# Kernel tuning notes

Hardware: AMD Instinct MI355X
Metric: run time of the kernel (lower is better)

## Reference

```python
import jax, jax.numpy as jnp
import numpy as np

EPS = 1e-6  # module eps (unused in forward math, kept for fidelity)


def _relative_transform(rot_a, trans_a, rot_b, trans_b):
    # rel_rot = R_a @ R_b^T ; rel_trans = t_a - rel_rot @ t_b
    rel_rot = jnp.einsum('bij,bkj->bik', rot_a, rot_b)          # [B,3,3]
    rel_trans = trans_a - jnp.einsum('bij,bj->bi', rel_rot, trans_b)  # [B,3]
    return rel_rot, rel_trans


def setup_inputs() -> dict:
    key = jax.random.key(0)
    ks = jax.random.split(key, 9)
    B, N = 8, 4096
    return {
        'pred_rot': jax.random.normal(ks[0], (B, 3, 3), jnp.float32),
        'pred_trans': jax.random.normal(ks[1], (B, 3), jnp.float32),
        'ctx_hyp_rot': jax.random.normal(ks[2], (B, 3, 3), jnp.float32),
        'ctx_hyp_trans': jax.random.normal(ks[3], (B, 3), jnp.float32),
        'gt_rot': jax.random.normal(ks[4], (B, 3, 3), jnp.float32),
        'gt_trans': jax.random.normal(ks[5], (B, 3), jnp.float32),
        'ctx_gt_rot': jax.random.normal(ks[6], (B, 3, 3), jnp.float32),
        'ctx_gt_trans': jax.random.normal(ks[7], (B, 3), jnp.float32),
        'model_points': jax.random.normal(ks[8], (B, N, 3), jnp.float32),
    }


def reference(pred_rot, pred_trans, ctx_hyp_rot, ctx_hyp_trans,
              gt_rot, gt_trans, ctx_gt_rot, ctx_gt_trans, model_points):
    rel_pred_rot, rel_pred_trans = _relative_transform(pred_rot, pred_trans, ctx_hyp_rot, ctx_hyp_trans)
    rel_gt_rot, rel_gt_trans = _relative_transform(gt_rot, gt_trans, ctx_gt_rot, ctx_gt_trans)

    # pts = P @ R^T + t   -> [B,N,3]
    pts_pred = jnp.einsum('bnj,bij->bni', model_points, rel_pred_rot) + rel_pred_trans[:, None, :]
    pts_gt = jnp.einsum('bnj,bij->bni', model_points, rel_gt_rot) + rel_gt_trans[:, None, :]

    # pairwise euclidean distance [B,N,M]
    sq = (jnp.sum(pts_pred**2, -1)[:, :, None]
          + jnp.sum(pts_gt**2, -1)[:, None, :]
          - 2.0 * jnp.einsum('bnd,bmd->bnm', pts_pred, pts_gt))
    dist = jnp.sqrt(jnp.maximum(sq, 0.0))

    # symmetric chamfer: mean of row-min + mean of col-min, per batch
    loss_geo = jnp.min(dist, axis=2).mean(axis=1) + jnp.min(dist, axis=1).mean(axis=1)  # [B]
    loss_trans = jnp.abs(rel_pred_trans - rel_gt_trans).mean()
    return (loss_geo.mean(), loss_trans)
```

## Files before the change

kernel.cpp:

```cpp
#include <hip/hip_runtime.h>
#include <math.h>


#define PTPB 256
#define CW    4
#define SA    2
#define CHUNK 32

typedef __attribute__((ext_vector_type(8)))  short bf16x8;
typedef __attribute__((ext_vector_type(16))) float f32x16;

__device__ __forceinline__ unsigned short f2bf(float x) {
    unsigned u = __float_as_uint(x);
    return (unsigned short)((u + 0x7FFFu + ((u >> 16) & 1u)) >> 16);
}
__device__ __forceinline__ float bf2f(unsigned short h) {
    return __uint_as_float(((unsigned)h) << 16);
}
__device__ __forceinline__ uint4 pack8(const unsigned short v[8]) {
    uint4 r;
    r.x = (unsigned)v[0] | ((unsigned)v[1] << 16);
    r.y = (unsigned)v[2] | ((unsigned)v[3] << 16);
    r.z = (unsigned)v[4] | ((unsigned)v[5] << 16);
    r.w = (unsigned)v[6] | ((unsigned)v[7] << 16);
    return r;
}
__device__ __forceinline__ float min3f(float a, float b, float c) {
    float d;
    asm("v_min3_f32 %0, %1, %2, %3" : "=v"(d) : "v"(a), "v"(b), "v"(c));
    return d;
}

__device__ __forceinline__ void rel_tf(const float* __restrict__ Ra,
                                       const float* __restrict__ ta,
                                       const float* __restrict__ Rb,
                                       const float* __restrict__ tb,
                                       float* R, float* t) {
#pragma unroll
    for (int i = 0; i < 3; i++)
#pragma unroll
        for (int k = 0; k < 3; k++)
            R[i * 3 + k] = Ra[i * 3 + 0] * Rb[k * 3 + 0]
                         + Ra[i * 3 + 1] * Rb[k * 3 + 1]
                         + Ra[i * 3 + 2] * Rb[k * 3 + 2];
#pragma unroll
    for (int i = 0; i < 3; i++)
        t[i] = ta[i] - (R[i * 3 + 0] * tb[0] + R[i * 3 + 1] * tb[1]
                      + R[i * 3 + 2] * tb[2]);
}

__global__ void k_prep(const float* __restrict__ pred_rot,
                       const float* __restrict__ pred_trans,
                       const float* __restrict__ ctx_hyp_rot,
                       const float* __restrict__ ctx_hyp_trans,
                       const float* __restrict__ gt_rot,
                       const float* __restrict__ gt_trans,
                       const float* __restrict__ ctx_gt_rot,
                       const float* __restrict__ ctx_gt_trans,
                       const float* __restrict__ mp,
                       uint4* __restrict__ Arow, uint4* __restrict__ Bcol,
                       float* __restrict__ pw,
                       float* __restrict__ out, int B, int N) {
    int idx = blockIdx.x * blockDim.x + threadIdx.x;
    if (idx >= B * N) return;
    int b = idx / N, n = idx % N;
    int T = N >> 5;
    int tile = n >> 5, ln = n & 31;
    float px = mp[idx * 3 + 0], py = mp[idx * 3 + 1], pz = mp[idx * 3 + 2];
    const unsigned short one = 0x3F80;
    float Rm[9], tv[3];
#pragma unroll
    for (int s = 0; s < 2; s++) {
        if (s == 0)
            rel_tf(pred_rot + b * 9, pred_trans + b * 3,
                   ctx_hyp_rot + b * 9, ctx_hyp_trans + b * 3, Rm, tv);
        else
            rel_tf(gt_rot + b * 9, gt_trans + b * 3,
                   ctx_gt_rot + b * 9, ctx_gt_trans + b * 3, Rm, tv);
        float x = Rm[0] * px + Rm[1] * py + Rm[2] * pz + tv[0];
        float y = Rm[3] * px + Rm[4] * py + Rm[5] * pz + tv[1];
        float z = Rm[6] * px + Rm[7] * py + Rm[8] * pz + tv[2];
        float w = x * x + y * y + z * z;

        float mx = -2.0f * x, my = -2.0f * y, mz = -2.0f * z;
        unsigned short ahx = f2bf(mx), ahy = f2bf(my), ahz = f2bf(mz);
        unsigned short alx = f2bf(mx - bf2f(ahx));
        unsigned short aly = f2bf(my - bf2f(ahy));
        unsigned short alz = f2bf(mz - bf2f(ahz));
        unsigned short ghx = f2bf(x), ghy = f2bf(y), ghz = f2bf(z);
        unsigned short glx = f2bf(x - bf2f(ghx));
        unsigned short gly = f2bf(y - bf2f(ghy));
        unsigned short glz = f2bf(z - bf2f(ghz));
        unsigned short gwh = f2bf(w);
        unsigned short gwl = f2bf(w - bf2f(gwh));

        unsigned short a_lo[8] = {ahx, ahy, ahz, alx, aly, alz, ahx, ahy};
        unsigned short a_hi[8] = {ahz, alx, aly, alz, one, one, 0, 0};
        unsigned short b_lo[8] = {ghx, ghy, ghz, ghx, ghy, ghz, glx, gly};
        unsigned short b_hi[8] = {glz, glx, gly, glz, gwh, gwl, 0, 0};

        size_t base = (((size_t)s * B + b) * T + tile) * 64;
        Arow[base + ln]      = pack8(a_lo);
        Arow[base + 32 + ln] = pack8(a_hi);
        Bcol[base + ln]      = pack8(b_lo);
        Bcol[base + 32 + ln] = pack8(b_hi);
        pw[((size_t)s * B + b) * N + n] = w;
    }
    if (idx == 0) {
        out[0] = 0.0f;
        float lt = 0.0f;
        for (int bb = 0; bb < B; bb++) {
            float Rp[9], tp[3], Rg[9], tg[3];
            rel_tf(pred_rot + bb * 9, pred_trans + bb * 3,
                   ctx_hyp_rot + bb * 9, ctx_hyp_trans + bb * 3, Rp, tp);
            rel_tf(gt_rot + bb * 9, gt_trans + bb * 3,
                   ctx_gt_rot + bb * 9, ctx_gt_trans + bb * 3, Rg, tg);
            lt += fabsf(tp[0] - tg[0]) + fabsf(tp[1] - tg[1]) + fabsf(tp[2] - tg[2]);
        }
        out[1] = lt / (float)(3 * B);
    }
}

__global__ void __launch_bounds__(CW * 64)
k_mfma(const uint4* __restrict__ Arow, const uint4* __restrict__ Bcol,
       const float* __restrict__ pw, float* __restrict__ out, int B, int N) {
    int T = N >> 5;
    int pass = blockIdx.z, b = blockIdx.y;
    int tid = threadIdx.x, wid = tid >> 6, lane = tid & 63;
    int strip0 = (blockIdx.x * CW + wid) * SA;

    const uint4* Ap  = Arow + ((size_t)pass * B + b) * T * 64;
    const uint4* Bs  = Bcol + ((size_t)(pass ^ 1) * B + b) * T * 64;
    const float* pwp = pw + ((size_t)pass * B + b) * N;

    __shared__ uint4 sB[CHUNK * 64];

    uint4 au0 = Ap[(size_t)strip0 * 64 + lane];
    uint4 au1 = Ap[(size_t)(strip0 + 1) * 64 + lane];
    bf16x8 af0 = *(bf16x8*)&au0;
    bf16x8 af1 = *(bf16x8*)&au1;

    f32x16 rmin0, rmin1, zc;
#pragma unroll
    for (int r = 0; r < 16; r++) { rmin0[r] = INFINITY; rmin1[r] = INFINITY; zc[r] = 0.0f; }

    int nch = T / CHUNK;
    uint4 stg[8];
#pragma unroll
    for (int i = 0; i < 8; i++) stg[i] = Bs[i * (CW * 64) + tid];

    for (int c = 0; c < nch; c++) {
        __syncthreads();
#pragma unroll
        for (int i = 0; i < 8; i++) sB[i * (CW * 64) + tid] = stg[i];
        __syncthreads();
        if (c + 1 < nch) {
#pragma unroll
            for (int i = 0; i < 8; i++)
                stg[i] = Bs[(size_t)(c + 1) * CHUNK * 64 + i * (CW * 64) + tid];
        }
#pragma unroll 4
        for (int t = 0; t < CHUNK; t += 2) {
            uint4 bu0 = sB[t * 64 + lane];
            uint4 bu1 = sB[(t + 1) * 64 + lane];
            bf16x8 bf0 = *(bf16x8*)&bu0;
            bf16x8 bf1 = *(bf16x8*)&bu1;
            f32x16 d00 = __builtin_amdgcn_mfma_f32_32x32x16_bf16(af0, bf0, zc, 0, 0, 0);
            f32x16 d01 = __builtin_amdgcn_mfma_f32_32x32x16_bf16(af0, bf1, zc, 0, 0, 0);
            f32x16 d10 = __builtin_amdgcn_mfma_f32_32x32x16_bf16(af1, bf0, zc, 0, 0, 0);
            f32x16 d11 = __builtin_amdgcn_mfma_f32_32x32x16_bf16(af1, bf1, zc, 0, 0, 0);
#pragma unroll
            for (int r = 0; r < 16; r++) {
                rmin0[r] = min3f(rmin0[r], d00[r], d01[r]);
                rmin1[r] = min3f(rmin1[r], d10[r], d11[r]);
            }
        }
    }

#pragma unroll
    for (int off = 1; off < 32; off <<= 1) {
#pragma unroll
        for (int r = 0; r < 16; r++) {
            rmin0[r] = fminf(rmin0[r], __shfl_xor(rmin0[r], off, 64));
            rmin1[r] = fminf(rmin1[r], __shfl_xor(rmin1[r], off, 64));
        }
    }

    float lsum = 0.0f;
    if ((lane & 31) == 0) {
        int h = lane >> 5;
        int rb0 = strip0 * 32, rb1 = rb0 + 32;
#pragma unroll
        for (int r = 0; r < 16; r++) {
            int row = (r & 3) + 8 * (r >> 2) + 4 * h;
            lsum += sqrtf(fmaxf(rmin0[r] + pwp[rb0 + row], 0.0f));
            lsum += sqrtf(fmaxf(rmin1[r] + pwp[rb1 + row], 0.0f));
        }
    }
    lsum += __shfl_down(lsum, 32, 64);

    __shared__ float red[CW];
    if (lane == 0) red[wid] = lsum;
    __syncthreads();
    if (tid == 0) {
        float tsum = 0.0f;
#pragma unroll
        for (int w = 0; w < CW; w++) tsum += red[w];
        atomicAdd(&out[0], tsum / (float)(B * N));
    }
}

extern "C" void kernel_launch(void* const* d_in, const int* in_sizes, int n_in,
                              void* d_out, int out_size, void* d_ws, size_t ws_size,
                              hipStream_t stream) {
    const float* pred_rot      = (const float*)d_in[0];
    const float* pred_trans    = (const float*)d_in[1];
    const float* ctx_hyp_rot   = (const float*)d_in[2];
    const float* ctx_hyp_trans = (const float*)d_in[3];
    const float* gt_rot        = (const float*)d_in[4];
    const float* gt_trans      = (const float*)d_in[5];
    const float* ctx_gt_rot    = (const float*)d_in[6];
    const float* ctx_gt_trans  = (const float*)d_in[7];
    const float* model_points  = (const float*)d_in[8];

    int B = in_sizes[0] / 9;
    int N = in_sizes[8] / (3 * B);
    int T = N >> 5;
    size_t fragN = (size_t)2 * B * T * 64;

    char* ws = (char*)d_ws;
    uint4* Arow = (uint4*)ws;
    uint4* Bcol = Arow + fragN;
    float* pw   = (float*)(Bcol + fragN);
    float* out  = (float*)d_out;

    k_prep<<<(B * N + PTPB - 1) / PTPB, PTPB, 0, stream>>>(
        pred_rot, pred_trans, ctx_hyp_rot, ctx_hyp_trans,
        gt_rot, gt_trans, ctx_gt_rot, ctx_gt_trans,
        model_points, Arow, Bcol, pw, out, B, N);

    dim3 grid(N / (CW * SA * 32), B, 2);
    k_mfma<<<grid, CW * 64, 0, stream>>>(Arow, Bcol, pw, out, B, N);
}
```

Baseline: 113.5 us.

## Split column range across wave pairs and merge row-mins through shared memory

Each block now has 8 waves instead of 4. Two waves share the same pair of row strips, and each scans half of the column tiles. Their partial row minima are merged through shared memory before the sqrt and sum. The shared-memory staging chunk is reorganised so each wave half reads its own column half. The change drops the inline v_min3 asm in favour of nested fminf and splits the four MFMAs into two pairs to reduce register pressure. It trades more waves per problem, for latency hiding, against an extra shared-memory reduction and more sync.

```diff
diff --git a/kernel.cpp b/kernel.cpp
--- a/kernel.cpp
+++ b/kernel.cpp
@@ -3,9 +3,8 @@
 
 
 #define PTPB 256
-#define CW    4
-#define SA    2
-#define CHUNK 32
+#define NW   8
+#define CH   16
 
 typedef __attribute__((ext_vector_type(8)))  short bf16x8;
 typedef __attribute__((ext_vector_type(16))) float f32x16;
@@ -24,11 +23,6 @@
     r.z = (unsigned)v[4] | ((unsigned)v[5] << 16);
     r.w = (unsigned)v[6] | ((unsigned)v[7] << 16);
     return r;
-}
-__device__ __forceinline__ float min3f(float a, float b, float c) {
-    float d;
-    asm("v_min3_f32 %0, %1, %2, %3" : "=v"(d) : "v"(a), "v"(b), "v"(c));
-    return d;
 }
 
 __device__ __forceinline__ void rel_tf(const float* __restrict__ Ra,
@@ -121,22 +115,27 @@
     }
 }
 
-__global__ void __launch_bounds__(CW * 64)
+__global__ void __launch_bounds__(NW * 64, 2)
 k_mfma(const uint4* __restrict__ Arow, const uint4* __restrict__ Bcol,
        const float* __restrict__ pw, float* __restrict__ out, int B, int N) {
     int T = N >> 5;
+    int T2 = T >> 1;
     int pass = blockIdx.z, b = blockIdx.y;
     int tid = threadIdx.x, wid = tid >> 6, lane = tid & 63;
-    int strip0 = (blockIdx.x * CW + wid) * SA;
+    int sp = wid >> 1;
+    int hcol = wid & 1;
+    int stripG = blockIdx.x * 8 + sp * 2;
 
     const uint4* Ap  = Arow + ((size_t)pass * B + b) * T * 64;
     const uint4* Bs  = Bcol + ((size_t)(pass ^ 1) * B + b) * T * 64;
     const float* pwp = pw + ((size_t)pass * B + b) * N;
 
-    __shared__ uint4 sB[CHUNK * 64];
-
-    uint4 au0 = Ap[(size_t)strip0 * 64 + lane];
-    uint4 au1 = Ap[(size_t)(strip0 + 1) * 64 + lane];
+    __shared__ uint4 sB[2 * CH * 64];
+    __shared__ float sRM[NW][2][2][16];
+    __shared__ float red[NW / 2];
+
+    uint4 au0 = Ap[(size_t)stripG * 64 + lane];
+    uint4 au1 = Ap[(size_t)(stripG + 1) * 64 + lane];
     bf16x8 af0 = *(bf16x8*)&au0;
     bf16x8 af1 = *(bf16x8*)&au1;
 
@@ -144,36 +143,44 @@
 #pragma unroll
     for (int r = 0; r < 16; r++) { rmin0[r] = INFINITY; rmin1[r] = INFINITY; zc[r] = 0.0f; }
 
-    int nch = T / CHUNK;
-    uint4 stg[8];
-#pragma unroll
-    for (int i = 0; i < 8; i++) stg[i] = Bs[i * (CW * 64) + tid];
+    int nch = T2 / CH;
+    uint4 stg[4];
+#pragma unroll
+    for (int k = 0; k < 4; k++) {
+        int j = tid + k * 512;
+        int hh = j >> 10, ti = (j & 1023) >> 6, el = j & 63;
+        stg[k] = Bs[((size_t)hh * T2 + ti) * 64 + el];
+    }
 
     for (int c = 0; c < nch; c++) {
         __syncthreads();
 #pragma unroll
-        for (int i = 0; i < 8; i++) sB[i * (CW * 64) + tid] = stg[i];
+        for (int k = 0; k < 4; k++) sB[tid + k * 512] = stg[k];
         __syncthreads();
         if (c + 1 < nch) {
 #pragma unroll
-            for (int i = 0; i < 8; i++)
-                stg[i] = Bs[(size_t)(c + 1) * CHUNK * 64 + i * (CW * 64) + tid];
-        }
-#pragma unroll 4
-        for (int t = 0; t < CHUNK; t += 2) {
-            uint4 bu0 = sB[t * 64 + lane];
-            uint4 bu1 = sB[(t + 1) * 64 + lane];
+            for (int k = 0; k < 4; k++) {
+                int j = tid + k * 512;
+                int hh = j >> 10, ti = (j & 1023) >> 6, el = j & 63;
+                stg[k] = Bs[((size_t)hh * T2 + (c + 1) * CH + ti) * 64 + el];
+            }
+        }
+        const uint4* sBh = sB + hcol * CH * 64;
+        for (int t = 0; t < CH; t += 2) {
+            uint4 bu0 = sBh[t * 64 + lane];
+            uint4 bu1 = sBh[(t + 1) * 64 + lane];
             bf16x8 bf0 = *(bf16x8*)&bu0;
             bf16x8 bf1 = *(bf16x8*)&bu1;
-            f32x16 d00 = __builtin_amdgcn_mfma_f32_32x32x16_bf16(af0, bf0, zc, 0, 0, 0);
-            f32x16 d01 = __builtin_amdgcn_mfma_f32_32x32x16_bf16(af0, bf1, zc, 0, 0, 0);
-            f32x16 d10 = __builtin_amdgcn_mfma_f32_32x32x16_bf16(af1, bf0, zc, 0, 0, 0);
-            f32x16 d11 = __builtin_amdgcn_mfma_f32_32x32x16_bf16(af1, bf1, zc, 0, 0, 0);
-#pragma unroll
-            for (int r = 0; r < 16; r++) {
-                rmin0[r] = min3f(rmin0[r], d00[r], d01[r]);
-                rmin1[r] = min3f(rmin1[r], d10[r], d11[r]);
-            }
+            f32x16 d0 = __builtin_amdgcn_mfma_f32_32x32x16_bf16(af0, bf0, zc, 0, 0, 0);
+            f32x16 d1 = __builtin_amdgcn_mfma_f32_32x32x16_bf16(af0, bf1, zc, 0, 0, 0);
+#pragma unroll
+            for (int r = 0; r < 16; r++)
+                rmin0[r] = fminf(fminf(rmin0[r], d0[r]), d1[r]);
+            d0 = __builtin_amdgcn_mfma_f32_32x32x16_bf16(af1, bf0, zc, 0, 0, 0);
+            d1 = __builtin_amdgcn_mfma_f32_32x32x16_bf16(af1, bf1, zc, 0, 0, 0);
+#pragma unroll
+            for (int r = 0; r < 16; r++)
+                rmin1[r] = fminf(fminf(rmin1[r], d0[r]), d1[r]);
         }
     }
 
@@ -185,29 +192,32 @@
             rmin1[r] = fminf(rmin1[r], __shfl_xor(rmin1[r], off, 64));
         }
     }
-
-    float lsum = 0.0f;
     if ((lane & 31) == 0) {
         int h = lane >> 5;
-        int rb0 = strip0 * 32, rb1 = rb0 + 32;
 #pragma unroll
         for (int r = 0; r < 16; r++) {
-            int row = (r & 3) + 8 * (r >> 2) + 4 * h;
-            lsum += sqrtf(fmaxf(rmin0[r] + pwp[rb0 + row], 0.0f));
-            lsum += sqrtf(fmaxf(rmin1[r] + pwp[rb1 + row], 0.0f));
-        }
-    }
-    lsum += __shfl_down(lsum, 32, 64);
-
-    __shared__ float red[CW];
-    if (lane == 0) red[wid] = lsum;
+            sRM[wid][0][h][r] = rmin0[r];
+            sRM[wid][1][h][r] = rmin1[r];
+        }
+    }
     __syncthreads();
-    if (tid == 0) {
-        float tsum = 0.0f;
-#pragma unroll
-        for (int w = 0; w < CW; w++) tsum += red[w];
-        atomicAdd(&out[0], tsum / (float)(B * N));
-    }
+
+    float s = 0.0f;
+    if (tid < 256) {
+        int lr = tid;
+        int strip = lr >> 5, rr = lr & 31;
+        int wa = (strip >> 1) * 2, sa = strip & 1;
+        int h = (rr >> 2) & 1;
+        int r = ((rr >> 3) << 2) | (rr & 3);
+        float v = fminf(sRM[wa][sa][h][r], sRM[wa + 1][sa][h][r]);
+        s = sqrtf(fmaxf(v + pwp[blockIdx.x * 256 + lr], 0.0f));
+    }
+#pragma unroll
+    for (int off = 32; off > 0; off >>= 1) s += __shfl_down(s, off, 64);
+    if (lane == 0 && wid < 4) red[wid] = s;
+    __syncthreads();
+    if (tid == 0)
+        atomicAdd(&out[0], (red[0] + red[1] + red[2] + red[3]) / (float)(B * N));
 }
 
 extern "C" void kernel_launch(void* const* d_in, const int* in_sizes, int n_in,
@@ -239,6 +249,6 @@
         gt_rot, gt_trans, ctx_gt_rot, ctx_gt_trans,
         model_points, Arow, Bcol, pw, out, B, N);
 
-    dim3 grid(N / (CW * SA * 32), B, 2);
-    k_mfma<<<grid, CW * 64, 0, stream>>>(Arow, Bcol, pw, out, B, N);
-}
+    dim3 grid((N >> 5) / 8, B, 2);
+    k_mfma<<<grid, NW * 64, 0, stream>>>(Arow, Bcol, pw, out, B, N);
+}
```

New measurement: 103.3 us. 1.1x faster.
